# Performance work log

Measured on AMD Instinct MI355X. Metric: run time of the kernel, lower is better.

## Reference

```python
import jax, jax.numpy as jnp
import numpy as np

B, D_IN, D_H, D_OUT, D_INT = 1024, 2048, 4096, 2048, 1024


def fwht(x):
    """Fast Walsh-Hadamard transform over a length-2^k vector (unnormalized),
    faithful to the torch chunk/cat butterfly loop."""
    n = x.shape[0]
    k = int(n).bit_length() - 1
    for i in range(k):
        y = x.reshape(2 ** i, 2, -1)        # split butterfly level i
        x = jnp.stack([y[:, 0] + y[:, 1], y[:, 0] - y[:, 1]], axis=1)
    return x.reshape(n)


def fastfood(V, BB, Pi, GG, DD):
    """fastfood_torched: pad -> B*x -> H -> permute -> G* -> H -> slice/scale."""
    LL = BB.shape[0]
    vpad = jnp.zeros((LL,), V.dtype).at[: V.shape[0]].set(V)
    m5 = fwht(fwht(BB * vpad)[Pi] * GG)
    divisor = jnp.sqrt(LL * jnp.sum(GG * GG))
    return m5[:DD] / (divisor * np.sqrt(float(DD) / LL))


def _ff_vars(key, DD):
    LL = 1 << int(np.ceil(np.log2(DD)))
    k1, k2, k3 = jax.random.split(key, 3)
    BB = jnp.where(jax.random.uniform(k1, (LL,)) < 0.5, -1.0, 1.0).astype(jnp.float32)
    Pi = jax.random.permutation(k2, LL).astype(jnp.int32)
    GG = jax.random.normal(k3, (LL,), dtype=jnp.float32)
    return BB, Pi, GG


def setup_inputs():
    key = jax.random.key(0)
    ks = jax.random.split(key, 8)
    x = jax.random.normal(ks[0], (B, D_IN), dtype=jnp.float32)
    V = jax.random.normal(ks[1], (D_INT,), dtype=jnp.float32) * 0.01
    W1_0 = jax.random.normal(ks[2], (D_H, D_IN), dtype=jnp.float32) * 0.02
    b1_0 = jnp.zeros((D_H,), jnp.float32)
    W2_0 = jax.random.normal(ks[3], (D_OUT, D_H), dtype=jnp.float32) * 0.02
    b2_0 = jnp.zeros((D_OUT,), jnp.float32)
    BB_W1, Pi_W1, GG_W1 = _ff_vars(ks[4], D_H * D_IN)
    BB_b1, Pi_b1, GG_b1 = _ff_vars(ks[5], D_H)
    BB_W2, Pi_W2, GG_W2 = _ff_vars(ks[6], D_OUT * D_H)
    BB_b2, Pi_b2, GG_b2 = _ff_vars(ks[7], D_OUT)
    return dict(x=x, V=V, W1_0=W1_0, b1_0=b1_0, W2_0=W2_0, b2_0=b2_0,
                BB_W1=BB_W1, Pi_W1=Pi_W1, GG_W1=GG_W1,
                BB_b1=BB_b1, Pi_b1=Pi_b1, GG_b1=GG_b1,
                BB_W2=BB_W2, Pi_W2=Pi_W2, GG_W2=GG_W2,
                BB_b2=BB_b2, Pi_b2=Pi_b2, GG_b2=GG_b2)


def reference(x, V, W1_0, b1_0, W2_0, b2_0,
              BB_W1, Pi_W1, GG_W1, BB_b1, Pi_b1, GG_b1,
              BB_W2, Pi_W2, GG_W2, BB_b2, Pi_b2, GG_b2):
    # Reconstruct each parameter: theta = theta0 + fastfood(V).view(shape)
    W1 = W1_0 + fastfood(V, BB_W1, Pi_W1, GG_W1, D_H * D_IN).reshape(D_H, D_IN)
    b1 = b1_0 + fastfood(V, BB_b1, Pi_b1, GG_b1, D_H)
    W2 = W2_0 + fastfood(V, BB_W2, Pi_W2, GG_W2, D_OUT * D_H).reshape(D_OUT, D_H)
    b2 = b2_0 + fastfood(V, BB_b2, Pi_b2, GG_b2, D_OUT)
    # Wrapped module forward (2-layer MLP)
    h = jax.nn.relu(x @ W1.T + b1)
    return h @ W2.T + b2
```

## Files before the change

kernel.cpp:

```cpp
#include <hip/hip_runtime.h>
#include <hip/hip_bf16.h>
#include <stdint.h>


typedef __attribute__((ext_vector_type(8))) short bf16x8;
typedef __attribute__((ext_vector_type(4))) float f32x4;

__device__ __forceinline__ ushort f2bf(float f) {
  union { float f; uint32_t u; } v; v.f = f;
  return (ushort)((v.u + 0x7FFFu + ((v.u >> 16) & 1u)) >> 16);
}
__device__ __forceinline__ float bf2f(ushort u) {
  union { uint32_t u; float f; } v; v.u = (uint32_t)u << 16; return v.f;
}

__device__ __forceinline__ void gload_lds16(const void* g, void* l) {
  __builtin_amdgcn_global_load_lds(
      (const __attribute__((address_space(1))) void*)g,
      (__attribute__((address_space(3))) void*)l, 16, 0, 0);
}

__device__ __forceinline__ void wait_vm16() { asm volatile("s_waitcnt vmcnt(16)" ::: "memory"); }
__device__ __forceinline__ void wait_vm8()  { asm volatile("s_waitcnt vmcnt(8)"  ::: "memory"); }
__device__ __forceinline__ void wait_vm0()  { asm volatile("s_waitcnt vmcnt(0)"  ::: "memory"); }
__device__ __forceinline__ void wait_lgkm0(){ asm volatile("s_waitcnt lgkmcnt(0)" ::: "memory"); }
__device__ __forceinline__ void barrier_raw(){ asm volatile("s_barrier" ::: "memory"); }
__device__ __forceinline__ void lds_barrier() {
  wait_lgkm0();
  barrier_raw();
  __builtin_amdgcn_sched_barrier(0);
}

template <int NN>
__device__ __forceinline__ void wht_inreg(float* v) {
#pragma unroll
  for (int h = 1; h < NN; h <<= 1)
#pragma unroll
    for (int g = 0; g < NN; g += (h << 1))
#pragma unroll
      for (int k = 0; k < h; ++k) {
        float a = v[g + k], b = v[g + k + h];
        v[g + k] = a + b; v[g + k + h] = a - b;
      }
}

__global__ __launch_bounds__(256) void prep(
    const float4* __restrict__ x4, ushort4* __restrict__ xb4,
    const float* __restrict__ V,
    const float* __restrict__ BBW1, const float* __restrict__ BBW2,
    float* __restrict__ t1, float* __restrict__ t2,
    const float* __restrict__ BBb1, const int* __restrict__ Pib1,
    const float* __restrict__ GGb1, const float* __restrict__ b10,
    const float* __restrict__ BBb2, const int* __restrict__ Pib2,
    const float* __restrict__ GGb2, const float* __restrict__ b20,
    float* __restrict__ ob1, float* __restrict__ ob2) {
  __shared__ float ts[1024];
  __shared__ float zs[4096];
  __shared__ float red[4];
  const int bid = blockIdx.x;
  const int tid = threadIdx.x;

  if (bid < 2048) {
    int i = bid * 256 + tid;
    float4 v = x4[i];
    ushort4 o;
    o.x = f2bf(v.x); o.y = f2bf(v.y); o.z = f2bf(v.z); o.w = f2bf(v.w);
    xb4[i] = o;
    return;
  }

  if (bid < 2050) {
    const int which = bid - 2048;
    const float* BB = which ? BBW2 : BBW1;
    float* t = which ? t2 : t1;
    for (int i = tid; i < 1024; i += 256) ts[i] = BB[i] * V[i];
    for (int st = 0; st < 10; ++st) {
      int half = 1 << st;
      __syncthreads();
      for (int j = tid; j < 512; j += 256) {
        int p = ((j >> st) << (st + 1)) | (j & (half - 1));
        float a = ts[p], b = ts[p + half];
        ts[p] = a + b; ts[p + half] = a - b;
      }
    }
    __syncthreads();
    for (int i = tid; i < 1024; i += 256) t[i] = ts[i];
    return;
  }

  {
    const int which = bid - 2050;
    const int L = which ? 2048 : 4096;
    const float* BB = which ? BBb2 : BBb1;
    const int* Pi = which ? Pib2 : Pib1;
    const float* GG = which ? GGb2 : GGb1;
    const float* b0 = which ? b20 : b10;
    float* ob = which ? ob2 : ob1;

    for (int i = tid; i < 1024; i += 256) ts[i] = BB[i] * V[i];
    for (int st = 0; st < 10; ++st) {
      int half = 1 << st;
      __syncthreads();
      for (int j = tid; j < 512; j += 256) {
        int p = ((j >> st) << (st + 1)) | (j & (half - 1));
        float a = ts[p], b = ts[p + half];
        ts[p] = a + b; ts[p + half] = a - b;
      }
    }
    __syncthreads();
    float gsum = 0.f;
    for (int i = tid; i < L; i += 256) {
      int pi = Pi[i];
      float g = GG[i];
      gsum += g * g;
      zs[i] = ts[pi & 1023] * g;
    }
    for (int o = 32; o > 0; o >>= 1) gsum += __shfl_down(gsum, o);
    if ((tid & 63) == 0) red[tid >> 6] = gsum;
    __syncthreads();
    float ssum = red[0] + red[1] + red[2] + red[3];
    for (int st = 0; (1 << st) < L; ++st) {
      int half = 1 << st;
      __syncthreads();
      for (int j = tid; j < (L >> 1); j += 256) {
        int p = ((j >> st) << (st + 1)) | (j & (half - 1));
        float a = zs[p], b = zs[p + half];
        zs[p] = a + b; zs[p + half] = a - b;
      }
    }
    __syncthreads();
    float scale = rsqrtf((float)L * ssum);
    for (int i = tid; i < L; i += 256) ob[i] = b0[i] + zs[i] * scale;
  }
}

__device__ __forceinline__ void p1_load(const int* __restrict__ Pi,
                                        const float* __restrict__ GG,
                                        size_t base, int s, int4* p4, float4* g4) {
  const int4* Pi4 = (const int4*)(Pi + base);
  const float4* GG4 = (const float4*)(GG + base);
#pragma unroll
  for (int j = 0; j < 8; ++j) { p4[j] = Pi4[(s << 3) + j]; g4[j] = GG4[(s << 3) + j]; }
}

__device__ __forceinline__ float p1_gather(const float* ts, const int4* p4,
                                           const float4* g4, float* v) {
  float gsum = 0.f;
#pragma unroll
  for (int j = 0; j < 8; ++j) {
    gsum += g4[j].x * g4[j].x + g4[j].y * g4[j].y + g4[j].z * g4[j].z + g4[j].w * g4[j].w;
    v[4 * j + 0] = ts[p4[j].x & 1023] * g4[j].x;
    v[4 * j + 1] = ts[p4[j].y & 1023] * g4[j].y;
    v[4 * j + 2] = ts[p4[j].z & 1023] * g4[j].z;
    v[4 * j + 3] = ts[p4[j].w & 1023] * g4[j].w;
  }
  wht_inreg<32>(v);
  for (int o = 32; o > 0; o >>= 1) gsum += __shfl_down(gsum, o);
  return gsum;
}

__device__ __forceinline__ void p1_lds(
    float* zs, float* red, int tid, float* v, float gs,
    ushort* __restrict__ inter, size_t base,
    float* __restrict__ partials, int chunkIdx) {
  lds_barrier();
  if ((tid & 63) == 0) red[tid >> 6] = gs;
#pragma unroll
  for (int j = 0; j < 16; ++j) {
    float2 u; u.x = v[2 * j]; u.y = v[2 * j + 1];
    *(float2*)&zs[34 * tid + 2 * j] = u;
  }
  lds_barrier();
  if (tid == 0) partials[chunkIdx] = red[0] + red[1] + red[2] + red[3];

  {
    const int pb = (tid & 31) + 1088 * (tid >> 5);
#pragma unroll
    for (int r = 0; r < 32; ++r) v[r] = zs[pb + 34 * r];
    wht_inreg<32>(v);
#pragma unroll
    for (int r = 0; r < 32; ++r) zs[pb + 34 * r] = v[r];
  }
  lds_barrier();

  {
    const int pc = 4 * tid + 2 * (tid >> 3);
    float w[4][8];
#pragma unroll
    for (int r = 0; r < 8; ++r) {
      float2 u0 = *(const float2*)&zs[pc + 1088 * r];
      float2 u1 = *(const float2*)&zs[pc + 1088 * r + 2];
      w[0][r] = u0.x; w[1][r] = u0.y; w[2][r] = u1.x; w[3][r] = u1.y;
    }
#pragma unroll
    for (int k = 0; k < 4; ++k) wht_inreg<8>(w[k]);
    ushort* op = inter + base + 4 * tid;
#pragma unroll
    for (int r = 0; r < 8; ++r) {
      short4 o;
      o.x = (short)f2bf(w[0][r]); o.y = (short)f2bf(w[1][r]);
      o.z = (short)f2bf(w[2][r]); o.w = (short)f2bf(w[3][r]);
      *(short4*)&op[r << 10] = o;
    }
  }
}

__global__ __launch_bounds__(256) void ff_pass1(
    const int* __restrict__ Pi1, const float* __restrict__ GG1,
    const int* __restrict__ Pi2, const float* __restrict__ GG2,
    const float* __restrict__ t1, const float* __restrict__ t2,
    ushort* __restrict__ inter1, ushort* __restrict__ inter2,
    float* __restrict__ partials) {
  __shared__ float ts[1024];
  __shared__ float zs[8704];
  __shared__ float red[4];
  const int tid = threadIdx.x;
  const int wsel = blockIdx.x >> 8;
  const int b = blockIdx.x & 255;
  const int* Pi = wsel ? Pi2 : Pi1;
  const float* GG = wsel ? GG2 : GG1;
  const float* t = wsel ? t2 : t1;
  ushort* inter = wsel ? inter2 : inter1;
  const int c0 = b << 2;
  const int pbase = (wsel << 10) + c0;

  int4 pA[8]; float4 gA[8]; int4 pB[8]; float4 gB[8];
  for (int i = tid; i < 1024; i += 256) ts[i] = t[i];
  p1_load(Pi, GG, (size_t)(c0 + 0) << 13, tid, pA, gA);
  p1_load(Pi, GG, (size_t)(c0 + 1) << 13, tid, pB, gB);
  __syncthreads();

  float v[32];
  float gs;
  gs = p1_gather(ts, pA, gA, v);
  p1_load(Pi, GG, (size_t)(c0 + 2) << 13, tid, pA, gA);
  p1_lds(zs, red, tid, v, gs, inter, (size_t)(c0 + 0) << 13, partials, pbase + 0);
  gs = p1_gather(ts, pB, gB, v);
  p1_load(Pi, GG, (size_t)(c0 + 3) << 13, tid, pB, gB);
  p1_lds(zs, red, tid, v, gs, inter, (size_t)(c0 + 1) << 13, partials, pbase + 1);
  gs = p1_gather(ts, pA, gA, v);
  p1_lds(zs, red, tid, v, gs, inter, (size_t)(c0 + 2) << 13, partials, pbase + 2);
  gs = p1_gather(ts, pB, gB, v);
  p1_lds(zs, red, tid, v, gs, inter, (size_t)(c0 + 3) << 13, partials, pbase + 3);
}

__global__ __launch_bounds__(512) void ff_pass2(
    const ushort* __restrict__ inter1, const ushort* __restrict__ inter2,
    const float* __restrict__ W01, const float* __restrict__ W02,
    const float* __restrict__ partials,
    ushort* __restrict__ W1b, ushort* __restrict__ W2b) {
  __shared__ ushort tile[1024][34];
  __shared__ float red[8];
  const int tid = threadIdx.x;
  const int wsel = blockIdx.x >> 8;
  const int cb = (blockIdx.x & 255) << 5;
  const ushort* inter = wsel ? inter2 : inter1;
  const float* W0 = wsel ? W02 : W01;
  ushort* Wb = wsel ? W2b : W1b;

  float s = partials[(wsel << 10) + tid] + partials[(wsel << 10) + tid + 512];
  for (int o = 32; o > 0; o >>= 1) s += __shfl_down(s, o);
  if ((tid & 63) == 0) red[tid >> 6] = s;

  const int p = tid & 15;
  const int g = tid >> 4;
  const ushort* ip = inter + ((size_t)(g << 5) << 13) + cb + (p << 1);
  float va[32], vb[32];
#pragma unroll
  for (int r = 0; r < 32; ++r) {
    ushort2 u = *(const ushort2*)(ip + ((size_t)r << 13));
    va[r] = bf2f(u.x); vb[r] = bf2f(u.y);
  }
  wht_inreg<32>(va);
  wht_inreg<32>(vb);
#pragma unroll
  for (int r = 0; r < 32; ++r) {
    ushort2 u; u.x = f2bf(va[r]); u.y = f2bf(vb[r]);
    *(ushort2*)&tile[(g << 5) + r][p << 1] = u;
  }
  __syncthreads();
  float ssum = 0.f;
#pragma unroll
  for (int k = 0; k < 8; ++k) ssum += red[k];
  const float sc = rsqrtf(8388608.f * ssum);

  float wa[32], wb[32];
#pragma unroll
  for (int r = 0; r < 32; ++r) {
    ushort2 u = *(const ushort2*)&tile[g + (r << 5)][p << 1];
    wa[r] = bf2f(u.x); wb[r] = bf2f(u.y);
  }
  wht_inreg<32>(wa);
  wht_inreg<32>(wb);
#pragma unroll
  for (int r = 0; r < 32; ++r) {
    size_t m = (((size_t)(g + (r << 5))) << 13) + cb + (p << 1);
    float2 w0 = *(const float2*)(W0 + m);
    ushort2 u;
    u.x = f2bf(wa[r] * sc + w0.x);
    u.y = f2bf(wb[r] * sc + w0.y);
    *(ushort2*)(Wb + m) = u;
  }
}

template <int EPI, int NT>
__global__ __launch_bounds__(256) void gemm_bt(
    const ushort* __restrict__ A, const ushort* __restrict__ B,
    const float* __restrict__ bias, ushort* __restrict__ Cb, float* __restrict__ Cf,
    int M, int N, int K) {
  __shared__ ushort As[4][8192];
  __shared__ ushort Bs[4][8192];
  const int tid = threadIdx.x;
  const int w = tid >> 6, l = tid & 63;
  const int wr = w >> 1, wc = w & 1;
  const int brow = blockIdx.y << 7, bcol = blockIdx.x << 7;
  const int lrow = l >> 3;
  const int csrc = ((l & 7) ^ lrow) << 3;
  const int l15 = l & 15;
  const int x7 = l15 & 7;
  const int kb = blockIdx.z * (NT << 6);
  f32x4 acc[4][4] = {};

  const ushort* pa = A + (size_t)(brow + (w << 5) + lrow) * K + kb + csrc;
  const ushort* pb = B + (size_t)(bcol + (w << 5) + lrow) * K + kb + csrc;
  const size_t K8 = (size_t)K << 3;

#define STAGE(buf, tt)                                                      \
  {                                                                         \
    const ushort* qa = pa + ((tt) << 6);                                    \
    const ushort* qb = pb + ((tt) << 6);                                    \
    _Pragma("unroll")                                                       \
    for (int i = 0; i < 4; ++i) {                                           \
      gload_lds16(qa + K8 * i, &As[buf][(((w << 2) + i) << 9)]);            \
      gload_lds16(qb + K8 * i, &Bs[buf][(((w << 2) + i) << 9)]);            \
    }                                                                       \
  }

  STAGE(0, 0); STAGE(1, 1); STAGE(2, 2);
  for (int t = 0; t < NT; ++t) {
    if (t < NT - 2) wait_vm16();
    else if (t == NT - 2) wait_vm8();
    else wait_vm0();
    barrier_raw();
    if (t + 3 < NT) STAGE((t + 3) & 3, t + 3);
    const ushort* Acur = As[t & 3];
    const ushort* Bcur = Bs[t & 3];
    bf16x8 af[2][4], bfr[2][4];
#pragma unroll
    for (int kk = 0; kk < 2; ++kk) {
      int c8 = (kk << 2) + (l >> 4);
#pragma unroll
      for (int m = 0; m < 4; ++m)
        af[kk][m] = *(const bf16x8*)&Acur[(((wr << 6) + (m << 4) + l15) << 6) + ((c8 ^ x7) << 3)];
#pragma unroll
      for (int n = 0; n < 4; ++n)
        bfr[kk][n] = *(const bf16x8*)&Bcur[(((wc << 6) + (n << 4) + l15) << 6) + ((c8 ^ x7) << 3)];
    }
    wait_lgkm0();
#pragma unroll
    for (int kk = 0; kk < 2; ++kk)
#pragma unroll
      for (int m = 0; m < 4; ++m)
#pragma unroll
        for (int n = 0; n < 4; ++n)
          acc[m][n] = __builtin_amdgcn_mfma_f32_16x16x32_bf16(af[kk][m], bfr[kk][n], acc[m][n], 0, 0, 0);
  }
#undef STAGE

  if (EPI == 0) {
#pragma unroll
    for (int n = 0; n < 4; ++n) {
      int col = bcol + (wc << 6) + (n << 4) + l15;
      float bv = bias[col];
#pragma unroll
      for (int m = 0; m < 4; ++m) {
        int row0 = brow + (wr << 6) + (m << 4) + ((l >> 4) << 2);
#pragma unroll
        for (int j = 0; j < 4; ++j) {
          float vv = fmaxf(acc[m][n][j] + bv, 0.f);
          Cb[(size_t)(row0 + j) * N + col] = f2bf(vv);
        }
      }
    }
  } else {
    float* outp = Cf + (size_t)blockIdx.z * M * N;
#pragma unroll
    for (int n = 0; n < 4; ++n) {
      int col = bcol + (wc << 6) + (n << 4) + l15;
#pragma unroll
      for (int m = 0; m < 4; ++m) {
        int row0 = brow + (wr << 6) + (m << 4) + ((l >> 4) << 2);
#pragma unroll
        for (int j = 0; j < 4; ++j)
          outp[(size_t)(row0 + j) * N + col] = acc[m][n][j];
      }
    }
  }
}

__global__ __launch_bounds__(256) void reduce_out(
    const float4* __restrict__ P, const float* __restrict__ b2,
    float4* __restrict__ out) {
  int i = blockIdx.x * 256 + threadIdx.x;
  float4 a = P[i], b = P[i + 524288];
  const float4 bb = *(const float4*)(b2 + ((i & 511) << 2));
  float4 o;
  o.x = a.x + b.x + bb.x; o.y = a.y + b.y + bb.y;
  o.z = a.z + b.z + bb.z; o.w = a.w + b.w + bb.w;
  out[i] = o;
}

extern "C" void kernel_launch(void* const* d_in, const int* in_sizes, int n_in,
                              void* d_out, int out_size, void* d_ws, size_t ws_size,
                              hipStream_t stream) {
  const float* x     = (const float*)d_in[0];
  const float* V     = (const float*)d_in[1];
  const float* W1_0  = (const float*)d_in[2];
  const float* b1_0  = (const float*)d_in[3];
  const float* W2_0  = (const float*)d_in[4];
  const float* b2_0  = (const float*)d_in[5];
  const float* BB_W1 = (const float*)d_in[6];
  const int*   Pi_W1 = (const int*)d_in[7];
  const float* GG_W1 = (const float*)d_in[8];
  const float* BB_b1 = (const float*)d_in[9];
  const int*   Pi_b1 = (const int*)d_in[10];
  const float* GG_b1 = (const float*)d_in[11];
  const float* BB_W2 = (const float*)d_in[12];
  const int*   Pi_W2 = (const int*)d_in[13];
  const float* GG_W2 = (const float*)d_in[14];
  const float* BB_b2 = (const float*)d_in[15];
  const int*   Pi_b2 = (const int*)d_in[16];
  const float* GG_b2 = (const float*)d_in[17];
  float* out = (float*)d_out;

  const size_t MB = 1048576ull;
  char* ws = (char*)d_ws;
  ushort* inter1 = (ushort*)(ws);
  float*  P      = (float*)(ws);
  ushort* inter2 = (ushort*)(ws + 16 * MB);
  ushort* W1b    = (ushort*)(ws + 32 * MB);
  ushort* W2b    = (ushort*)(ws + 48 * MB);
  ushort* xb     = (ushort*)(ws + 64 * MB);
  ushort* hb     = (ushort*)(ws + 68 * MB);
  char*   S      = ws + 76 * MB;
  float*  t1     = (float*)(S);
  float*  t2     = (float*)(S + 4096);
  float*  b1     = (float*)(S + 8192);
  float*  b2     = (float*)(S + 8192 + 16384);
  float*  parts  = (float*)(S + 8192 + 16384 + 8192);

  prep<<<2052, 256, 0, stream>>>((const float4*)x, (ushort4*)xb, V,
                                 BB_W1, BB_W2, t1, t2,
                                 BB_b1, Pi_b1, GG_b1, b1_0,
                                 BB_b2, Pi_b2, GG_b2, b2_0, b1, b2);

  ff_pass1<<<512, 256, 0, stream>>>(Pi_W1, GG_W1, Pi_W2, GG_W2, t1, t2,
                                    inter1, inter2, parts);
  ff_pass2<<<512, 512, 0, stream>>>(inter1, inter2, W1_0, W2_0, parts, W1b, W2b);

  gemm_bt<0, 32><<<dim3(32, 8, 1), 256, 0, stream>>>(xb, W1b, b1, hb, nullptr, 1024, 4096, 2048);
  gemm_bt<1, 32><<<dim3(16, 8, 2), 256, 0, stream>>>(hb, W2b, nullptr, nullptr, P, 1024, 2048, 4096);
  reduce_out<<<2048, 256, 0, stream>>>((const float4*)P, b2, (float4*)out);
}
```

Baseline: 172.9 us.

## Split fastfood gather and first WHT stage into two separate kernels

The fused, software-pipelined ff_pass1 kernel is replaced by two kernels. build_z does the permuted gather times GG, writes the result as bf16 to a new intermediate buffer, and reduces the GG partial sums. wht13 then reads that buffer back and runs the 32x8x32 in-register/LDS Hadamard stages. Each kernel launches 2048 blocks that handle one chunk each, which gives more parallelism and lighter per-thread register use. The cost is an extra full round trip of the intermediate through global memory, one more launch, and rounding to bf16 before the transform, which adds numerical error.

New measurement: 176.6 us. 2.2% more time.

```diff
diff --git a/kernel.cpp b/kernel.cpp
--- a/kernel.cpp
+++ b/kernel.cpp
@@ -4,6 +4,7 @@
 
 
 typedef __attribute__((ext_vector_type(8))) short bf16x8;
+typedef __attribute__((ext_vector_type(8))) short short8;
 typedef __attribute__((ext_vector_type(4))) float f32x4;
 
 __device__ __forceinline__ ushort f2bf(float f) {
@@ -25,11 +26,6 @@
 __device__ __forceinline__ void wait_vm0()  { asm volatile("s_waitcnt vmcnt(0)"  ::: "memory"); }
 __device__ __forceinline__ void wait_lgkm0(){ asm volatile("s_waitcnt lgkmcnt(0)" ::: "memory"); }
 __device__ __forceinline__ void barrier_raw(){ asm volatile("s_barrier" ::: "memory"); }
-__device__ __forceinline__ void lds_barrier() {
-  wait_lgkm0();
-  barrier_raw();
-  __builtin_amdgcn_sched_barrier(0);
-}
 
 template <int NN>
 __device__ __forceinline__ void wht_inreg(float* v) {
@@ -134,44 +130,86 @@
   }
 }
 
-__device__ __forceinline__ void p1_load(const int* __restrict__ Pi,
-                                        const float* __restrict__ GG,
-                                        size_t base, int s, int4* p4, float4* g4) {
+__global__ __launch_bounds__(256) void build_z(
+    const int* __restrict__ Pi1, const float* __restrict__ GG1,
+    const int* __restrict__ Pi2, const float* __restrict__ GG2,
+    const float* __restrict__ t1, const float* __restrict__ t2,
+    ushort* __restrict__ z1, ushort* __restrict__ z2,
+    float* __restrict__ partials) {
+  __shared__ float ts[1024];
+  __shared__ float red[4];
+  const int tid = threadIdx.x;
+  const int wsel = blockIdx.x >> 10;
+  const int blk = blockIdx.x & 1023;
+  const int* __restrict__ Pi = wsel ? Pi2 : Pi1;
+  const float* __restrict__ GG = wsel ? GG2 : GG1;
+  const float* t = wsel ? t2 : t1;
+  ushort* __restrict__ z = wsel ? z2 : z1;
+  const size_t base = (size_t)blk << 13;
+
+  for (int i = tid; i < 1024; i += 256) ts[i] = t[i];
+
+  int4 p4[8]; float4 g4[8];
   const int4* Pi4 = (const int4*)(Pi + base);
   const float4* GG4 = (const float4*)(GG + base);
 #pragma unroll
-  for (int j = 0; j < 8; ++j) { p4[j] = Pi4[(s << 3) + j]; g4[j] = GG4[(s << 3) + j]; }
-}
-
-__device__ __forceinline__ float p1_gather(const float* ts, const int4* p4,
-                                           const float4* g4, float* v) {
+  for (int q = 0; q < 4; ++q) {
+    p4[2 * q]     = Pi4[(q << 9) + (tid << 1)];
+    p4[2 * q + 1] = Pi4[(q << 9) + (tid << 1) + 1];
+    g4[2 * q]     = GG4[(q << 9) + (tid << 1)];
+    g4[2 * q + 1] = GG4[(q << 9) + (tid << 1) + 1];
+  }
+  __syncthreads();
+
   float gsum = 0.f;
 #pragma unroll
-  for (int j = 0; j < 8; ++j) {
-    gsum += g4[j].x * g4[j].x + g4[j].y * g4[j].y + g4[j].z * g4[j].z + g4[j].w * g4[j].w;
-    v[4 * j + 0] = ts[p4[j].x & 1023] * g4[j].x;
-    v[4 * j + 1] = ts[p4[j].y & 1023] * g4[j].y;
-    v[4 * j + 2] = ts[p4[j].z & 1023] * g4[j].z;
-    v[4 * j + 3] = ts[p4[j].w & 1023] * g4[j].w;
+  for (int q = 0; q < 4; ++q) {
+    const int4 pa = p4[2 * q], pb = p4[2 * q + 1];
+    const float4 ga = g4[2 * q], gb = g4[2 * q + 1];
+    gsum += ga.x * ga.x + ga.y * ga.y + ga.z * ga.z + ga.w * ga.w
+          + gb.x * gb.x + gb.y * gb.y + gb.z * gb.z + gb.w * gb.w;
+    short8 o;
+    o[0] = (short)f2bf(ts[pa.x & 1023] * ga.x);
+    o[1] = (short)f2bf(ts[pa.y & 1023] * ga.y);
+    o[2] = (short)f2bf(ts[pa.z & 1023] * ga.z);
+    o[3] = (short)f2bf(ts[pa.w & 1023] * ga.w);
+    o[4] = (short)f2bf(ts[pb.x & 1023] * gb.x);
+    o[5] = (short)f2bf(ts[pb.y & 1023] * gb.y);
+    o[6] = (short)f2bf(ts[pb.z & 1023] * gb.z);
+    o[7] = (short)f2bf(ts[pb.w & 1023] * gb.w);
+    *(short8*)(z + base + (q << 11) + (tid << 3)) = o;
+  }
+  for (int o2 = 32; o2 > 0; o2 >>= 1) gsum += __shfl_down(gsum, o2);
+  if ((tid & 63) == 0) red[tid >> 6] = gsum;
+  __syncthreads();
+  if (tid == 0) partials[blockIdx.x] = red[0] + red[1] + red[2] + red[3];
+}
+
+__global__ __launch_bounds__(256) void wht13(
+    const ushort* __restrict__ zz1, const ushort* __restrict__ zz2,
+    ushort* __restrict__ inter1, ushort* __restrict__ inter2) {
+  __shared__ float zs[8704];
+  const int tid = threadIdx.x;
+  const int wsel = blockIdx.x >> 10;
+  const int blk = blockIdx.x & 1023;
+  const ushort* __restrict__ z = wsel ? zz2 : zz1;
+  ushort* __restrict__ inter = wsel ? inter2 : inter1;
+  const size_t base = (size_t)blk << 13;
+
+  float v[32];
+#pragma unroll
+  for (int j = 0; j < 4; ++j) {
+    short8 d = *(const short8*)(z + base + (tid << 5) + (j << 3));
+#pragma unroll
+    for (int k = 0; k < 8; ++k) v[(j << 3) + k] = bf2f((ushort)d[k]);
   }
   wht_inreg<32>(v);
-  for (int o = 32; o > 0; o >>= 1) gsum += __shfl_down(gsum, o);
-  return gsum;
-}
-
-__device__ __forceinline__ void p1_lds(
-    float* zs, float* red, int tid, float* v, float gs,
-    ushort* __restrict__ inter, size_t base,
-    float* __restrict__ partials, int chunkIdx) {
-  lds_barrier();
-  if ((tid & 63) == 0) red[tid >> 6] = gs;
 #pragma unroll
   for (int j = 0; j < 16; ++j) {
     float2 u; u.x = v[2 * j]; u.y = v[2 * j + 1];
     *(float2*)&zs[34 * tid + 2 * j] = u;
   }
-  lds_barrier();
-  if (tid == 0) partials[chunkIdx] = red[0] + red[1] + red[2] + red[3];
+  __syncthreads();
 
   {
     const int pb = (tid & 31) + 1088 * (tid >> 5);
@@ -181,7 +219,7 @@
 #pragma unroll
     for (int r = 0; r < 32; ++r) zs[pb + 34 * r] = v[r];
   }
-  lds_barrier();
+  __syncthreads();
 
   {
     const int pc = 4 * tid + 2 * (tid >> 3);
@@ -203,45 +241,6 @@
       *(short4*)&op[r << 10] = o;
     }
   }
-}
-
-__global__ __launch_bounds__(256) void ff_pass1(
-    const int* __restrict__ Pi1, const float* __restrict__ GG1,
-    const int* __restrict__ Pi2, const float* __restrict__ GG2,
-    const float* __restrict__ t1, const float* __restrict__ t2,
-    ushort* __restrict__ inter1, ushort* __restrict__ inter2,
-    float* __restrict__ partials) {
-  __shared__ float ts[1024];
-  __shared__ float zs[8704];
-  __shared__ float red[4];
-  const int tid = threadIdx.x;
-  const int wsel = blockIdx.x >> 8;
-  const int b = blockIdx.x & 255;
-  const int* Pi = wsel ? Pi2 : Pi1;
-  const float* GG = wsel ? GG2 : GG1;
-  const float* t = wsel ? t2 : t1;
-  ushort* inter = wsel ? inter2 : inter1;
-  const int c0 = b << 2;
-  const int pbase = (wsel << 10) + c0;
-
-  int4 pA[8]; float4 gA[8]; int4 pB[8]; float4 gB[8];
-  for (int i = tid; i < 1024; i += 256) ts[i] = t[i];
-  p1_load(Pi, GG, (size_t)(c0 + 0) << 13, tid, pA, gA);
-  p1_load(Pi, GG, (size_t)(c0 + 1) << 13, tid, pB, gB);
-  __syncthreads();
-
-  float v[32];
-  float gs;
-  gs = p1_gather(ts, pA, gA, v);
-  p1_load(Pi, GG, (size_t)(c0 + 2) << 13, tid, pA, gA);
-  p1_lds(zs, red, tid, v, gs, inter, (size_t)(c0 + 0) << 13, partials, pbase + 0);
-  gs = p1_gather(ts, pB, gB, v);
-  p1_load(Pi, GG, (size_t)(c0 + 3) << 13, tid, pB, gB);
-  p1_lds(zs, red, tid, v, gs, inter, (size_t)(c0 + 1) << 13, partials, pbase + 1);
-  gs = p1_gather(ts, pA, gA, v);
-  p1_lds(zs, red, tid, v, gs, inter, (size_t)(c0 + 2) << 13, partials, pbase + 2);
-  gs = p1_gather(ts, pB, gB, v);
-  p1_lds(zs, red, tid, v, gs, inter, (size_t)(c0 + 3) << 13, partials, pbase + 3);
 }
 
 __global__ __launch_bounds__(512) void ff_pass2(
@@ -438,6 +437,8 @@
   ushort* inter1 = (ushort*)(ws);
   float*  P      = (float*)(ws);
   ushort* inter2 = (ushort*)(ws + 16 * MB);
+  ushort* z1     = (ushort*)(ws + 32 * MB);
+  ushort* z2     = (ushort*)(ws + 48 * MB);
   ushort* W1b    = (ushort*)(ws + 32 * MB);
   ushort* W2b    = (ushort*)(ws + 48 * MB);
   ushort* xb     = (ushort*)(ws + 64 * MB);
@@ -454,8 +455,9 @@
                                  BB_b1, Pi_b1, GG_b1, b1_0,
                                  BB_b2, Pi_b2, GG_b2, b2_0, b1, b2);
 
-  ff_pass1<<<512, 256, 0, stream>>>(Pi_W1, GG_W1, Pi_W2, GG_W2, t1, t2,
-                                    inter1, inter2, parts);
+  build_z<<<2048, 256, 0, stream>>>(Pi_W1, GG_W1, Pi_W2, GG_W2, t1, t2,
+                                    z1, z2, parts);
+  wht13<<<2048, 256, 0, stream>>>(z1, z2, inter1, inter2);
   ff_pass2<<<512, 512, 0, stream>>>(inter1, inter2, W1_0, W2_0, parts, W1b, W2b);
 
   gemm_bt<0, 32><<<dim3(32, 8, 1), 256, 0, stream>>>(xb, W1b, b1, hb, nullptr, 1024, 4096, 2048);
```
